# Kernel optimization log

Measured on AMD Instinct MI355X. Metric: run time of the kernel, lower is better.

Reference implementation:

```python
import jax, jax.numpy as jnp
import numpy as np

DIM = 384
NUM_HEADS = 12
HEAD_DIM = 32
MID = NUM_HEADS * HEAD_DIM
RES = (32, 32)


def _relative_position_index(res):
    Hh, Ww = res
    coords = np.stack(np.meshgrid(np.arange(Hh), np.arange(Ww), indexing='ij'))  # 2,H,W
    cf = coords.reshape(2, -1)
    rel = cf[:, :, None] - cf[:, None, :]  # 2,N,N
    rel = rel.transpose(1, 2, 0).astype(np.int64)
    rel[:, :, 0] += Hh - 1
    rel[:, :, 1] += Ww - 1
    rel[:, :, 0] *= 2 * Ww - 1
    return rel.sum(-1)  # N,N


def setup_inputs() -> dict:
    key = jax.random.key(0)
    ks = jax.random.split(key, 8)
    B = 8
    Hh, Ww = RES
    table_size = (2 * Hh - 1) * (2 * Ww - 1)
    x = jax.random.normal(ks[0], (B, DIM, Hh, Ww), dtype=jnp.float32)
    wq = jax.random.normal(ks[1], (MID, DIM), dtype=jnp.float32) * 0.02
    bq = jnp.zeros((MID,), dtype=jnp.float32)
    wkv = jax.random.normal(ks[2], (2 * MID, DIM), dtype=jnp.float32) * 0.02
    bkv = jnp.zeros((2 * MID,), dtype=jnp.float32)
    wproj = jax.random.normal(ks[3], (DIM, MID), dtype=jnp.float32) * 0.02
    bproj = jnp.zeros((DIM,), dtype=jnp.float32)
    bias_table = jax.random.normal(ks[4], (table_size, NUM_HEADS), dtype=jnp.float32) * 0.02
    rel_index = jnp.asarray(_relative_position_index(RES), dtype=jnp.int32)  # N,N
    return {"x": x, "wq": wq, "bq": bq, "wkv": wkv, "bkv": bkv,
            "wproj": wproj, "bproj": bproj, "bias_table": bias_table,
            "rel_index": rel_index}


def reference(x, wq, bq, wkv, bkv, wproj, bproj, bias_table, rel_index):
    B, C, Hh, Ww = x.shape
    N = Hh * Ww
    scale = HEAD_DIM ** -0.5
    xf = x.reshape(B, C, N)  # B,C,N
    # 1x1 convs == channelwise linear
    q = jnp.einsum('oc,bcn->bon', wq, xf) + bq[None, :, None]          # B,MID,N
    kv = jnp.einsum('oc,bcn->bon', wkv, xf) + bkv[None, :, None]       # B,2*MID,N
    q = q.reshape(B, NUM_HEADS, HEAD_DIM, N).transpose(0, 1, 3, 2)     # B,h,N,d
    kv = kv.reshape(B, 2, NUM_HEADS, HEAD_DIM, N)
    k = kv[:, 0].transpose(0, 1, 3, 2)                                  # B,h,N,d
    v = kv[:, 1].transpose(0, 1, 3, 2)                                  # B,h,N,d
    attn = jnp.einsum('bhnd,bhmd->bhnm', q, k) * scale                  # B,h,N,N
    rel_bias = bias_table[rel_index.reshape(-1)].reshape(N, N, NUM_HEADS)
    attn = attn + rel_bias.transpose(2, 0, 1)[None]                     # + h,N,N bias
    attn = jax.nn.softmax(attn, axis=-1)
    out = jnp.einsum('bhnm,bhmd->bhnd', attn, v)                        # B,h,N,d
    out = out.transpose(0, 1, 3, 2).reshape(B, MID, N)                  # B,MID,N
    out = jnp.einsum('om,bmn->bon', wproj, out) + bproj[None, :, None]  # B,DIM,N
    return out.reshape(B, C, Hh, Ww)
```

## Files before the change

kernel.cpp:

```cpp
#include <hip/hip_runtime.h>

typedef __bf16 bf16;
typedef __bf16 bf16x8 __attribute__((ext_vector_type(8)));
typedef __bf16 bf16x4 __attribute__((ext_vector_type(4)));
typedef float  f32x4  __attribute__((ext_vector_type(4)));

static constexpr int NB = 8;
static constexpr int NH = 12;
static constexpr int HD = 32;
static constexpr int NN = 1024;
static constexpr int NC = 384;

static constexpr float LOG2E = 1.4426950408889634f;
static constexpr float QSC   = (float)(0.17677669529663687 * 1.4426950408889634);

static constexpr size_t XT_N   = (size_t)NB*NN*NC;
static constexpr size_t WQKV_N = (size_t)3*NC*NC;
static constexpr size_t WP_N   = (size_t)NC*NC;
static constexpr size_t QKV_N  = (size_t)NB*NH*NN*HD;
static constexpr size_t AO_N   = (size_t)NB*NN*NC;

static constexpr size_t XT_OFF   = 0;
static constexpr size_t WQKV_OFF = XT_OFF + XT_N;
static constexpr size_t WP_OFF   = WQKV_OFF + WQKV_N;
static constexpr size_t Q_OFF    = WP_OFF + WP_N;
static constexpr size_t K_OFF    = Q_OFF + QKV_N;
static constexpr size_t V_OFF    = K_OFF + QKV_N;
static constexpr size_t AO_OFF   = V_OFF + QKV_N;
static constexpr size_t PT_OFF   = AO_OFF + AO_N;

static constexpr int PT_PER_H = 63 * 62;
static constexpr int PT_TOTAL = NH * PT_PER_H;

#define MFMA16(a,b,c) __builtin_amdgcn_mfma_f32_16x16x32_bf16(a,b,c,0,0,0)

static __device__ inline float fast_exp2(float x) {
#if __has_builtin(__builtin_amdgcn_exp2f)
    return __builtin_amdgcn_exp2f(x);
#else
    return exp2f(x);
#endif
}

__global__ __launch_bounds__(256) void cast_all_kernel(const float* __restrict__ x,
                                                       const float* __restrict__ wq,
                                                       const float* __restrict__ wkv,
                                                       const float* __restrict__ wproj,
                                                       const float* __restrict__ bias_table,
                                                       bf16* __restrict__ xt,
                                                       bf16* __restrict__ wqkv,
                                                       bf16* __restrict__ wp,
                                                       unsigned* __restrict__ PT)
{
    __shared__ bf16 T[64][68];
    const int t = threadIdx.x;
    if (blockIdx.x >= 1344) {
        const int e = (blockIdx.x - 1344) * 256 + t;
        if (e >= PT_TOTAL) return;
        const int h = e / PT_PER_H, rem = e - h * PT_PER_H;
        const int dj = rem / 62, dip = rem - dj * 62;
        bf16 lo = (bf16)(bias_table[(size_t)((dip + 1) * 63 + dj) * NH + h] * LOG2E);
        bf16 hi = (bf16)(bias_table[(size_t)(dip * 63 + dj) * NH + h] * LOG2E);
        PT[e] = (unsigned)__builtin_bit_cast(unsigned short, lo)
              | ((unsigned)__builtin_bit_cast(unsigned short, hi) << 16);
        return;
    }
    if (blockIdx.x >= 768) {
        const size_t i = ((size_t)(blockIdx.x - 768) * 256 + t) * 4;
        if (i >= WQKV_N + WP_N) return;
        const float* src; bf16* dst;
        if (i < (size_t)NC*NC)      { src = wq + i;                     dst = wqkv + i; }
        else if (i < WQKV_N)        { src = wkv + (i - (size_t)NC*NC);  dst = wqkv + i; }
        else                        { src = wproj + (i - WQKV_N);       dst = wp + (i - WQKV_N); }
        float4 v = *(const float4*)src;
        bf16x4 o; o[0] = (bf16)v.x; o[1] = (bf16)v.y; o[2] = (bf16)v.z; o[3] = (bf16)v.w;
        *(bf16x4*)dst = o;
        return;
    }
    const int bid = blockIdx.x;
    const int b = bid / 96, rem = bid % 96, ct = rem >> 4, nt = rem & 15;
    const int c0 = ct * 64, n0 = nt * 64;
    const float* Xb = x + (size_t)b * NC * NN;
    const int nl = t & 63, c4 = (t >> 6) * 4;
#pragma unroll
    for (int i = 0; i < 4; ++i) {
        const int c = c4 + i * 16;
        bf16x4 v;
#pragma unroll
        for (int j = 0; j < 4; ++j)
            v[j] = (bf16)Xb[(size_t)(c0 + c + j) * NN + n0 + nl];
        *(bf16x4*)&T[nl][c] = v;
    }
    __syncthreads();
    const int n = t >> 2;
#pragma unroll
    for (int i = 0; i < 2; ++i) {
        const int cg = (t & 3) * 8 + i * 32;
        bf16x4 a = *(const bf16x4*)&T[n][cg];
        bf16x4 bv = *(const bf16x4*)&T[n][cg + 4];
        bf16x8 vv = __builtin_shufflevector(a, bv, 0, 1, 2, 3, 4, 5, 6, 7);
        *(bf16x8*)&xt[((size_t)b * NN + n0 + n) * NC + c0 + cg] = vv;
    }
}

__global__ __launch_bounds__(256) void qkv_gemm_kernel(
    const bf16* __restrict__ W, const bf16* __restrict__ Xt,
    const float* __restrict__ bq, const float* __restrict__ bkv,
    bf16* __restrict__ Qd, bf16* __restrict__ Kd, bf16* __restrict__ Vd)
{
    __shared__ bf16 As[128][72];
    __shared__ bf16 Bs[128][72];
    const int t = threadIdx.x;
    const int w = t >> 6, lane = t & 63, g = lane >> 4, l16 = lane & 15;
    const int wm = w >> 1, wn = w & 1;
    const int n0g = blockIdx.x * 128;
    const int b = n0g >> 10, n0 = n0g & 1023;
    const int o0 = blockIdx.y * 128;
    const bf16* Xb = Xt + (size_t)b * NN * NC;

    const int sr = t >> 1, sc2 = (t & 1) * 32;

    f32x4 acc[4][4] = {};

    bf16x8 aw[4], bw[4];
#pragma unroll
    for (int i = 0; i < 4; ++i) {
        aw[i] = *(const bf16x8*)&W [(size_t)(o0 + sr) * NC + sc2 + 8*i];
        bw[i] = *(const bf16x8*)&Xb[(size_t)(n0 + sr) * NC + sc2 + 8*i];
    }

    for (int k0 = 0; k0 < NC; k0 += 64) {
        __syncthreads();
#pragma unroll
        for (int i = 0; i < 4; ++i) {
            *(bf16x8*)&As[sr][sc2 + 8*i] = aw[i];
            *(bf16x8*)&Bs[sr][sc2 + 8*i] = bw[i];
        }
        __syncthreads();
        if (k0 + 64 < NC) {
#pragma unroll
            for (int i = 0; i < 4; ++i) {
                aw[i] = *(const bf16x8*)&W [(size_t)(o0 + sr) * NC + k0 + 64 + sc2 + 8*i];
                bw[i] = *(const bf16x8*)&Xb[(size_t)(n0 + sr) * NC + k0 + 64 + sc2 + 8*i];
            }
        }
#pragma unroll
        for (int ks = 0; ks < 2; ++ks) {
            bf16x8 a[4], bb[4];
#pragma unroll
            for (int s = 0; s < 4; ++s) {
                a[s]  = *(const bf16x8*)&As[wm*64 + s*16 + l16][ks*32 + g*8];
                bb[s] = *(const bf16x8*)&Bs[wn*64 + s*16 + l16][ks*32 + g*8];
            }
#pragma unroll
            for (int sm = 0; sm < 4; ++sm)
#pragma unroll
                for (int sn = 0; sn < 4; ++sn)
                    acc[sm][sn] = MFMA16(a[sm], bb[sn], acc[sm][sn]);
        }
    }

#pragma unroll
    for (int sm = 0; sm < 4; ++sm)
#pragma unroll
    for (int sn = 0; sn < 4; ++sn) {
        const int col   = n0 + wn*64 + sn*16 + l16;
        const int obase = o0 + wm*64 + sm*16 + g*4;
        f32x4 v = acc[sm][sn];
        if (obase < 384) {
            const int hh = obase >> 5, d = obase & 31;
            bf16x4 o4;
#pragma unroll
            for (int r = 0; r < 4; ++r) o4[r] = (bf16)((v[r] + bq[obase + r]) * QSC);
            *(bf16x4*)&Qd[(((size_t)b*NH + hh)*NN + col)*HD + d] = o4;
        } else if (obase < 768) {
            const int oo = obase - 384; const int hh = oo >> 5, d = oo & 31;
            bf16x4 o4;
#pragma unroll
            for (int r = 0; r < 4; ++r) o4[r] = (bf16)(v[r] + bkv[oo + r]);
            *(bf16x4*)&Kd[(((size_t)b*NH + hh)*NN + col)*HD + d] = o4;
        } else {
            const int oo = obase - 768; const int hh = oo >> 5, d = oo & 31;
#pragma unroll
            for (int r = 0; r < 4; ++r)
                Vd[(((size_t)b*NH + hh)*HD + d + r)*NN + col] = (bf16)(v[r] + bkv[obase - 384 + r]);
        }
    }
}

__global__ __launch_bounds__(256, 4) void attn_kernel(
    const bf16* __restrict__ Qg, const bf16* __restrict__ Kg, const bf16* __restrict__ Vg,
    const unsigned* __restrict__ PT, bf16* __restrict__ AOt)
{
    __shared__ unsigned int pairTw[63][34];
    __shared__ bf16 Ks[128][40];
    __shared__ bf16 Vs[2][32][72];

    const int t = threadIdx.x;
    const int w = t >> 6, lane = t & 63, g = lane >> 4, l16 = lane & 15;

    const int bid = blockIdx.x;
    const int nid = (bid & 7) * 96 + (bid >> 3);
    const int qt = nid & 7;
    const int hb = nid >> 3;
    const int h = hb % 12, b = hb / 12;

    const bf16* Qb = Qg + ((size_t)(b*NH + h)) * NN * HD;
    const bf16* Kb = Kg + ((size_t)(b*NH + h)) * NN * HD;
    const bf16* Vb = Vg + ((size_t)(b*NH + h)) * HD * NN;

    const int kr = t >> 1, kc2 = (t & 1) * 16;
    const int vd = t >> 3, vmb = (t & 7) * 16;
    int vsub[2], vqa[2];
#pragma unroll
    for (int i = 0; i < 2; ++i) {
        const int vm = vmb + 8*i, vmm = vm & 63;
        vsub[i] = vm >> 6;
        vqa[i]  = ((vmm >> 5) & 1) * 32 + ((vmm >> 2) & 3) * 8 + ((vmm >> 4) & 1) * 4;
    }

    bf16x8 sregK[2], sregV[2];
#pragma unroll
    for (int i = 0; i < 2; ++i) {
        sregK[i] = *(const bf16x8*)&Kb[(size_t)kr * HD + kc2 + 8*i];
        sregV[i] = *(const bf16x8*)&Vb[(size_t)vd * NN + vmb + 8*i];
    }

    const int q0 = qt * 128;
    const bf16x8 qfrag0 = *(const bf16x8*)&Qb[(size_t)(q0 + w*32      + l16) * HD + g*8];
    const bf16x8 qfrag1 = *(const bf16x8*)&Qb[(size_t)(q0 + w*32 + 16 + l16) * HD + g*8];

    const unsigned* PTh = PT + (size_t)h * PT_PER_H + 4 * qt;
    for (int idx = t; idx < 63 * 34; idx += 256) {
        const int dj = idx / 34, dipl = idx - dj * 34;
        pairTw[dj][dipl] = PTh[dj * 62 + dipl];
    }

    const unsigned* twp = &pairTw[0][0];
    const int rowD1 = (l16 + 31 - 4*g) * 34;

    bf16x8 vones;
#pragma unroll
    for (int e = 0; e < 8; ++e) vones[e] = (bf16)1.0f;

    f32x4 oacc0[2] = {}, oacc1[2] = {};
    f32x4 oacc_l0 = {}, oacc_l1 = {};

    for (int ph = 0; ph < 8; ++ph) {
        __syncthreads();
#pragma unroll
        for (int i = 0; i < 2; ++i) {
            *(bf16x8*)&Ks[kr][kc2 + 8*i] = sregK[i];
            bf16x4 vlo = __builtin_shufflevector(sregV[i], sregV[i], 0, 1, 2, 3);
            bf16x4 vhi = __builtin_shufflevector(sregV[i], sregV[i], 4, 5, 6, 7);
            *(bf16x4*)&Vs[vsub[i]][vd][vqa[i]]     = vlo;
            *(bf16x4*)&Vs[vsub[i]][vd][vqa[i] + 8] = vhi;
        }
        __syncthreads();
        if (ph < 7) {
            const int m1 = (ph + 1) * 128;
#pragma unroll
            for (int i = 0; i < 2; ++i) {
                sregK[i] = *(const bf16x8*)&Kb[(size_t)(m1 + kr) * HD + kc2 + 8*i];
                sregV[i] = *(const bf16x8*)&Vb[(size_t)vd * NN + m1 + vmb + 8*i];
            }
        }

#pragma unroll
        for (int sub = 0; sub < 2; ++sub) {
            const int it = 2 * ph + sub;
            const bf16 (*Vsp)[72] = Vs[sub];
            const int dipl = w + 30 - 2*it;
            const unsigned* pD1 = twp + rowD1 + dipl;

            f32x4 b00, b01, b02, b03, b10, b12;
#pragma unroll
            for (int r = 0; r < 4; ++r) {
                const unsigned d1w = pD1[-34 * r];
                const unsigned d0w = pD1[-34 * r - 544];
                const unsigned d2w = pD1[-34 * r + 544];
                b00[r] = __uint_as_float(d1w << 16);
                b02[r] = __uint_as_float(d1w & 0xFFFF0000u);
                b01[r] = __uint_as_float(d0w << 16);
                b03[r] = __uint_as_float(d0w & 0xFFFF0000u);
                b10[r] = __uint_as_float(d2w << 16);
                b12[r] = __uint_as_float(d2w & 0xFFFF0000u);
            }
            f32x4 bacc0[4] = {b00, b01, b02, b03};
            f32x4 bacc1[4] = {b10, b00, b12, b02};

            bf16x8 pa0[2], pa1[2];
#pragma unroll
            for (int sc = 0; sc < 4; ++sc) {
                bf16x8 kf = *(const bf16x8*)&Ks[sub*64 + sc*16 + l16][g*8];
                f32x4 z0 = MFMA16(kf, qfrag0, bacc0[sc]);
                f32x4 z1 = MFMA16(kf, qfrag1, bacc1[sc]);
                const int kc = sc >> 1, hl = (sc & 1) * 4;
#pragma unroll
                for (int r = 0; r < 4; ++r) {
                    pa0[kc][hl + r] = (bf16)fast_exp2(z0[r]);
                    pa1[kc][hl + r] = (bf16)fast_exp2(z1[r]);
                }
            }

#pragma unroll
            for (int kc = 0; kc < 2; ++kc) {
#pragma unroll
                for (int ds = 0; ds < 2; ++ds) {
                    bf16x8 vf = *(const bf16x8*)&Vsp[ds*16 + l16][kc*32 + 8*g];
                    oacc0[ds] = MFMA16(pa0[kc], vf, oacc0[ds]);
                    oacc1[ds] = MFMA16(pa1[kc], vf, oacc1[ds]);
                }
                oacc_l0 = MFMA16(pa0[kc], vones, oacc_l0);
                oacc_l1 = MFMA16(pa1[kc], vones, oacc_l1);
            }
        }
    }

    float rin0[4], rin1[4];
#pragma unroll
    for (int r = 0; r < 4; ++r) {
        rin0[r] = 1.0f / oacc_l0[r];
        rin1[r] = 1.0f / oacc_l1[r];
    }

    const int nrow0 = q0 + w*32 + g*4;
#pragma unroll
    for (int ds = 0; ds < 2; ++ds) {
        const int c = h*HD + ds*16 + l16;
#pragma unroll
        for (int r = 0; r < 4; ++r) {
            AOt[((size_t)b*NN + nrow0 + r)      * NC + c] = (bf16)(oacc0[ds][r] * rin0[r]);
            AOt[((size_t)b*NN + nrow0 + 16 + r) * NC + c] = (bf16)(oacc1[ds][r] * rin1[r]);
        }
    }
}

__global__ __launch_bounds__(256) void proj_gemm_kernel(
    const bf16* __restrict__ W, const bf16* __restrict__ AOt,
    const float* __restrict__ bproj, float* __restrict__ out)
{
    __shared__ bf16 As[64][40];
    __shared__ bf16 Bs[128][40];
    const int t = threadIdx.x;
    const int w = t >> 6, lane = t & 63, g = lane >> 4, l16 = lane & 15;
    const int wm = w >> 1, wn = w & 1;
    const int n0g = blockIdx.x * 128;
    const int b = n0g >> 10, n0 = n0g & 1023;
    const int o0 = blockIdx.y * 64;
    const bf16* Ab = AOt + (size_t)b * NN * NC;

    const int ar = t >> 2, ac = (t & 3) * 8;

    f32x4 acc[2][4] = {};

    bf16x8 aw = *(const bf16x8*)&W[(size_t)(o0 + ar) * NC + ac];
    bf16x8 bw[2];
#pragma unroll
    for (int i = 0; i < 2; ++i) {
        const int s = t + i * 256, r = s >> 2, cc = (s & 3) * 8;
        bw[i] = *(const bf16x8*)&Ab[(size_t)(n0 + r) * NC + cc];
    }

    for (int k0 = 0; k0 < NC; k0 += 32) {
        __syncthreads();
        *(bf16x8*)&As[ar][ac] = aw;
#pragma unroll
        for (int i = 0; i < 2; ++i) {
            const int s = t + i * 256, r = s >> 2, cc = (s & 3) * 8;
            *(bf16x8*)&Bs[r][cc] = bw[i];
        }
        __syncthreads();
        if (k0 + 32 < NC) {
            aw = *(const bf16x8*)&W[(size_t)(o0 + ar) * NC + k0 + 32 + ac];
#pragma unroll
            for (int i = 0; i < 2; ++i) {
                const int s = t + i * 256, r = s >> 2, cc = (s & 3) * 8;
                bw[i] = *(const bf16x8*)&Ab[(size_t)(n0 + r) * NC + k0 + 32 + cc];
            }
        }
        bf16x8 a0 = *(const bf16x8*)&As[wm*32      + l16][g*8];
        bf16x8 a1 = *(const bf16x8*)&As[wm*32 + 16 + l16][g*8];
#pragma unroll
        for (int sn = 0; sn < 4; ++sn) {
            bf16x8 bf = *(const bf16x8*)&Bs[wn*64 + sn*16 + l16][g*8];
            acc[0][sn] = MFMA16(a0, bf, acc[0][sn]);
            acc[1][sn] = MFMA16(a1, bf, acc[1][sn]);
        }
    }

#pragma unroll
    for (int sm = 0; sm < 2; ++sm)
#pragma unroll
    for (int sn = 0; sn < 4; ++sn) {
        const int col   = n0 + wn*64 + sn*16 + l16;
        const int obase = o0 + wm*32 + sm*16 + g*4;
        f32x4 v = acc[sm][sn];
#pragma unroll
        for (int r = 0; r < 4; ++r)
            out[((size_t)b*NC + obase + r)*NN + col] = v[r] + bproj[obase + r];
    }
}

extern "C" void kernel_launch(void* const* d_in, const int* in_sizes, int n_in,
                              void* d_out, int out_size, void* d_ws, size_t ws_size,
                              hipStream_t stream)
{
    const float* x          = (const float*)d_in[0];
    const float* wq         = (const float*)d_in[1];
    const float* bq         = (const float*)d_in[2];
    const float* wkv        = (const float*)d_in[3];
    const float* bkv        = (const float*)d_in[4];
    const float* wproj      = (const float*)d_in[5];
    const float* bproj      = (const float*)d_in[6];
    const float* bias_table = (const float*)d_in[7];
    float* out = (float*)d_out;

    bf16* wsb  = (bf16*)d_ws;
    bf16* Xt   = wsb + XT_OFF;
    bf16* Wqkv = wsb + WQKV_OFF;
    bf16* Wp   = wsb + WP_OFF;
    bf16* Qd   = wsb + Q_OFF;
    bf16* Kd   = wsb + K_OFF;
    bf16* Vd   = wsb + V_OFF;
    bf16* AOt  = wsb + AO_OFF;
    unsigned* PT = (unsigned*)(wsb + PT_OFF);

    const int ptBlocks = (PT_TOTAL + 255) / 256;
    cast_all_kernel<<<dim3(768 + 576 + ptBlocks), 256, 0, stream>>>(
        x, wq, wkv, wproj, bias_table, Xt, Wqkv, Wp, PT);
    qkv_gemm_kernel<<<dim3(64, 9), 256, 0, stream>>>(Wqkv, Xt, bq, bkv, Qd, Kd, Vd);
    attn_kernel<<<dim3(768), 256, 0, stream>>>(Qd, Kd, Vd, PT, AOt);
    proj_gemm_kernel<<<dim3(64, 6), 256, 0, stream>>>(Wp, AOt, bproj, out);
}
```

Baseline: 64.66 us.

## Split attention key range across two warp groups with LDS reduction

Measured after the change: 131.8 us. +103.8%, slower.

```diff
diff --git a/kernel.cpp b/kernel.cpp
--- a/kernel.cpp
+++ b/kernel.cpp
@@ -188,16 +188,18 @@
     }
 }
 
-__global__ __launch_bounds__(256, 4) void attn_kernel(
+__global__ __launch_bounds__(512, 6) void attn_kernel(
     const bf16* __restrict__ Qg, const bf16* __restrict__ Kg, const bf16* __restrict__ Vg,
     const unsigned* __restrict__ PT, bf16* __restrict__ AOt)
 {
-    __shared__ unsigned int pairTw[63][34];
-    __shared__ bf16 Ks[128][40];
-    __shared__ bf16 Vs[2][32][72];
+    __shared__ __align__(16) char arena[47488];
+    bf16 (*KsH)[128][40]   = (bf16 (*)[128][40])arena;
+    bf16 (*VsH)[2][32][72] = (bf16 (*)[2][32][72])(arena + 20480);
+    unsigned (*pairTw)[34] = (unsigned (*)[34])(arena + 38912);
 
     const int t = threadIdx.x;
     const int w = t >> 6, lane = t & 63, g = lane >> 4, l16 = lane & 15;
+    const int wl = w & 3, hf = w >> 2;
 
     const int bid = blockIdx.x;
     const int nid = (bid & 7) * 96 + (bid >> 3);
@@ -209,8 +211,9 @@
     const bf16* Kb = Kg + ((size_t)(b*NH + h)) * NN * HD;
     const bf16* Vb = Vg + ((size_t)(b*NH + h)) * HD * NN;
 
-    const int kr = t >> 1, kc2 = (t & 1) * 16;
-    const int vd = t >> 3, vmb = (t & 7) * 16;
+    const int tl = t & 255, g2 = t >> 8;
+    const int kr = tl >> 1, kc2 = (tl & 1) * 16;
+    const int vd = tl >> 3, vmb = (tl & 7) * 16;
     int vsub[2], vqa[2];
 #pragma unroll
     for (int i = 0; i < 2; ++i) {
@@ -218,20 +221,21 @@
         vsub[i] = vm >> 6;
         vqa[i]  = ((vmm >> 5) & 1) * 32 + ((vmm >> 2) & 3) * 8 + ((vmm >> 4) & 1) * 4;
     }
+    const int mbase = g2 * 512;
 
     bf16x8 sregK[2], sregV[2];
 #pragma unroll
     for (int i = 0; i < 2; ++i) {
-        sregK[i] = *(const bf16x8*)&Kb[(size_t)kr * HD + kc2 + 8*i];
-        sregV[i] = *(const bf16x8*)&Vb[(size_t)vd * NN + vmb + 8*i];
+        sregK[i] = *(const bf16x8*)&Kb[(size_t)(mbase + kr) * HD + kc2 + 8*i];
+        sregV[i] = *(const bf16x8*)&Vb[(size_t)vd * NN + mbase + vmb + 8*i];
     }
 
     const int q0 = qt * 128;
-    const bf16x8 qfrag0 = *(const bf16x8*)&Qb[(size_t)(q0 + w*32      + l16) * HD + g*8];
-    const bf16x8 qfrag1 = *(const bf16x8*)&Qb[(size_t)(q0 + w*32 + 16 + l16) * HD + g*8];
+    const bf16x8 qfrag0 = *(const bf16x8*)&Qb[(size_t)(q0 + wl*32      + l16) * HD + g*8];
+    const bf16x8 qfrag1 = *(const bf16x8*)&Qb[(size_t)(q0 + wl*32 + 16 + l16) * HD + g*8];
 
     const unsigned* PTh = PT + (size_t)h * PT_PER_H + 4 * qt;
-    for (int idx = t; idx < 63 * 34; idx += 256) {
+    for (int idx = t; idx < 63 * 34; idx += 512) {
         const int dj = idx / 34, dipl = idx - dj * 34;
         pairTw[dj][dipl] = PTh[dj * 62 + dipl];
     }
@@ -246,19 +250,19 @@
     f32x4 oacc0[2] = {}, oacc1[2] = {};
     f32x4 oacc_l0 = {}, oacc_l1 = {};
 
-    for (int ph = 0; ph < 8; ++ph) {
+    for (int ph = 0; ph < 4; ++ph) {
         __syncthreads();
 #pragma unroll
         for (int i = 0; i < 2; ++i) {
-            *(bf16x8*)&Ks[kr][kc2 + 8*i] = sregK[i];
+            *(bf16x8*)&KsH[g2][kr][kc2 + 8*i] = sregK[i];
             bf16x4 vlo = __builtin_shufflevector(sregV[i], sregV[i], 0, 1, 2, 3);
             bf16x4 vhi = __builtin_shufflevector(sregV[i], sregV[i], 4, 5, 6, 7);
-            *(bf16x4*)&Vs[vsub[i]][vd][vqa[i]]     = vlo;
-            *(bf16x4*)&Vs[vsub[i]][vd][vqa[i] + 8] = vhi;
-        }
-        __syncthreads();
-        if (ph < 7) {
-            const int m1 = (ph + 1) * 128;
+            *(bf16x4*)&VsH[g2][vsub[i]][vd][vqa[i]]     = vlo;
+            *(bf16x4*)&VsH[g2][vsub[i]][vd][vqa[i] + 8] = vhi;
+        }
+        __syncthreads();
+        if (ph < 3) {
+            const int m1 = mbase + (ph + 1) * 128;
 #pragma unroll
             for (int i = 0; i < 2; ++i) {
                 sregK[i] = *(const bf16x8*)&Kb[(size_t)(m1 + kr) * HD + kc2 + 8*i];
@@ -268,9 +272,9 @@
 
 #pragma unroll
         for (int sub = 0; sub < 2; ++sub) {
-            const int it = 2 * ph + sub;
-            const bf16 (*Vsp)[72] = Vs[sub];
-            const int dipl = w + 30 - 2*it;
+            const int it = hf * 8 + 2 * ph + sub;
+            const bf16 (*Vsp)[72] = VsH[hf][sub];
+            const int dipl = wl + 30 - 2*it;
             const unsigned* pD1 = twp + rowD1 + dipl;
 
             f32x4 b00, b01, b02, b03, b10, b12;
@@ -292,7 +296,7 @@
             bf16x8 pa0[2], pa1[2];
 #pragma unroll
             for (int sc = 0; sc < 4; ++sc) {
-                bf16x8 kf = *(const bf16x8*)&Ks[sub*64 + sc*16 + l16][g*8];
+                bf16x8 kf = *(const bf16x8*)&KsH[hf][sub*64 + sc*16 + l16][g*8];
                 f32x4 z0 = MFMA16(kf, qfrag0, bacc0[sc]);
                 f32x4 z1 = MFMA16(kf, qfrag1, bacc1[sc]);
                 const int kc = sc >> 1, hl = (sc & 1) * 4;
@@ -317,21 +321,35 @@
         }
     }
 
-    float rin0[4], rin1[4];
-#pragma unroll
-    for (int r = 0; r < 4; ++r) {
-        rin0[r] = 1.0f / oacc_l0[r];
-        rin1[r] = 1.0f / oacc_l1[r];
-    }
-
-    const int nrow0 = q0 + w*32 + g*4;
-#pragma unroll
-    for (int ds = 0; ds < 2; ++ds) {
-        const int c = h*HD + ds*16 + l16;
+    __syncthreads();
+    f32x4* mbuf = (f32x4*)arena;
+    const int sb = wl * 64 + lane;
+    if (hf == 1) {
+        mbuf[0*256 + sb] = oacc0[0]; mbuf[1*256 + sb] = oacc0[1];
+        mbuf[2*256 + sb] = oacc1[0]; mbuf[3*256 + sb] = oacc1[1];
+        mbuf[4*256 + sb] = oacc_l0;  mbuf[5*256 + sb] = oacc_l1;
+    }
+    __syncthreads();
+    if (hf == 0) {
+        oacc0[0] += mbuf[0*256 + sb]; oacc0[1] += mbuf[1*256 + sb];
+        oacc1[0] += mbuf[2*256 + sb]; oacc1[1] += mbuf[3*256 + sb];
+        oacc_l0  += mbuf[4*256 + sb]; oacc_l1  += mbuf[5*256 + sb];
+
+        float rin0[4], rin1[4];
 #pragma unroll
         for (int r = 0; r < 4; ++r) {
-            AOt[((size_t)b*NN + nrow0 + r)      * NC + c] = (bf16)(oacc0[ds][r] * rin0[r]);
-            AOt[((size_t)b*NN + nrow0 + 16 + r) * NC + c] = (bf16)(oacc1[ds][r] * rin1[r]);
+            rin0[r] = 1.0f / oacc_l0[r];
+            rin1[r] = 1.0f / oacc_l1[r];
+        }
+        const int nrow0 = q0 + wl*32 + g*4;
+#pragma unroll
+        for (int ds = 0; ds < 2; ++ds) {
+            const int c = h*HD + ds*16 + l16;
+#pragma unroll
+            for (int r = 0; r < 4; ++r) {
+                AOt[((size_t)b*NN + nrow0 + r)      * NC + c] = (bf16)(oacc0[ds][r] * rin0[r]);
+                AOt[((size_t)b*NN + nrow0 + 16 + r) * NC + c] = (bf16)(oacc1[ds][r] * rin1[r]);
+            }
         }
     }
 }
@@ -430,6 +448,6 @@
     cast_all_kernel<<<dim3(768 + 576 + ptBlocks), 256, 0, stream>>>(
         x, wq, wkv, wproj, bias_table, Xt, Wqkv, Wp, PT);
     qkv_gemm_kernel<<<dim3(64, 9), 256, 0, stream>>>(Wqkv, Xt, bq, bkv, Qd, Kd, Vd);
-    attn_kernel<<<dim3(768), 256, 0, stream>>>(Qd, Kd, Vd, PT, AOt);
+    attn_kernel<<<dim3(768), 512, 0, stream>>>(Qd, Kd, Vd, PT, AOt);
     proj_gemm_kernel<<<dim3(64, 6), 256, 0, stream>>>(Wp, AOt, bproj, out);
 }
```

## Drop LDS K/V staging in attention; read pre-permuted V directly from global

Applied to the files above, without the earlier changes.

Result: slower. 106.5 us (+64.7%).

```diff
diff --git a/kernel.cpp b/kernel.cpp
--- a/kernel.cpp
+++ b/kernel.cpp
@@ -181,9 +181,10 @@
             *(bf16x4*)&Kd[(((size_t)b*NH + hh)*NN + col)*HD + d] = o4;
         } else {
             const int oo = obase - 768; const int hh = oo >> 5, d = oo & 31;
+            const int pcol = (col & ~0x1C) | (((col >> 2) & 3) << 3) | (((col >> 4) & 1) << 2);
 #pragma unroll
             for (int r = 0; r < 4; ++r)
-                Vd[(((size_t)b*NH + hh)*HD + d + r)*NN + col] = (bf16)(v[r] + bkv[obase - 384 + r]);
+                Vd[(((size_t)b*NH + hh)*HD + d + r)*NN + pcol] = (bf16)(v[r] + bkv[obase - 384 + r]);
         }
     }
 }
@@ -192,147 +193,112 @@
     const bf16* __restrict__ Qg, const bf16* __restrict__ Kg, const bf16* __restrict__ Vg,
     const unsigned* __restrict__ PT, bf16* __restrict__ AOt)
 {
-    __shared__ unsigned int pairTw[63][34];
-    __shared__ bf16 Ks[128][40];
-    __shared__ bf16 Vs[2][32][72];
+    __shared__ unsigned pairTw[63][32];
 
     const int t = threadIdx.x;
     const int w = t >> 6, lane = t & 63, g = lane >> 4, l16 = lane & 15;
 
     const int bid = blockIdx.x;
-    const int nid = (bid & 7) * 96 + (bid >> 3);
-    const int qt = nid & 7;
-    const int hb = nid >> 3;
+    const int nid = (bid & 7) * 192 + (bid >> 3);
+    const int qt = nid & 15;
+    const int hb = nid >> 4;
     const int h = hb % 12, b = hb / 12;
 
     const bf16* Qb = Qg + ((size_t)(b*NH + h)) * NN * HD;
     const bf16* Kb = Kg + ((size_t)(b*NH + h)) * NN * HD;
     const bf16* Vb = Vg + ((size_t)(b*NH + h)) * HD * NN;
 
-    const int kr = t >> 1, kc2 = (t & 1) * 16;
-    const int vd = t >> 3, vmb = (t & 7) * 16;
-    int vsub[2], vqa[2];
-#pragma unroll
-    for (int i = 0; i < 2; ++i) {
-        const int vm = vmb + 8*i, vmm = vm & 63;
-        vsub[i] = vm >> 6;
-        vqa[i]  = ((vmm >> 5) & 1) * 32 + ((vmm >> 2) & 3) * 8 + ((vmm >> 4) & 1) * 4;
-    }
-
-    bf16x8 sregK[2], sregV[2];
-#pragma unroll
-    for (int i = 0; i < 2; ++i) {
-        sregK[i] = *(const bf16x8*)&Kb[(size_t)kr * HD + kc2 + 8*i];
-        sregV[i] = *(const bf16x8*)&Vb[(size_t)vd * NN + vmb + 8*i];
-    }
-
-    const int q0 = qt * 128;
-    const bf16x8 qfrag0 = *(const bf16x8*)&Qb[(size_t)(q0 + w*32      + l16) * HD + g*8];
-    const bf16x8 qfrag1 = *(const bf16x8*)&Qb[(size_t)(q0 + w*32 + 16 + l16) * HD + g*8];
-
-    const unsigned* PTh = PT + (size_t)h * PT_PER_H + 4 * qt;
-    for (int idx = t; idx < 63 * 34; idx += 256) {
-        const int dj = idx / 34, dipl = idx - dj * 34;
+    const int q0 = qt * 64;
+    const int n_s = q0 + w*16 + l16;
+    const bf16x8 qfrag = *(const bf16x8*)&Qb[(size_t)n_s * HD + g*8];
+
+    bf16x8 kf[2][4];
+#pragma unroll
+    for (int sc = 0; sc < 4; ++sc)
+        kf[0][sc] = *(const bf16x8*)&Kb[(size_t)(sc*16 + l16) * HD + g*8];
+
+    const unsigned* PTh = PT + (size_t)h * PT_PER_H + 2 * qt;
+    for (int idx = t; idx < 63 * 32; idx += 256) {
+        const int dj = idx >> 5, dipl = idx & 31;
         pairTw[dj][dipl] = PTh[dj * 62 + dipl];
     }
+    __syncthreads();
 
     const unsigned* twp = &pairTw[0][0];
-    const int rowD1 = (l16 + 31 - 4*g) * 34;
+    const int rowD1 = ((((w & 1) << 4) | l16) + 31 - 4*g) * 32;
 
     bf16x8 vones;
 #pragma unroll
     for (int e = 0; e < 8; ++e) vones[e] = (bf16)1.0f;
 
-    f32x4 oacc0[2] = {}, oacc1[2] = {};
-    f32x4 oacc_l0 = {}, oacc_l1 = {};
-
-    for (int ph = 0; ph < 8; ++ph) {
-        __syncthreads();
-#pragma unroll
-        for (int i = 0; i < 2; ++i) {
-            *(bf16x8*)&Ks[kr][kc2 + 8*i] = sregK[i];
-            bf16x4 vlo = __builtin_shufflevector(sregV[i], sregV[i], 0, 1, 2, 3);
-            bf16x4 vhi = __builtin_shufflevector(sregV[i], sregV[i], 4, 5, 6, 7);
-            *(bf16x4*)&Vs[vsub[i]][vd][vqa[i]]     = vlo;
-            *(bf16x4*)&Vs[vsub[i]][vd][vqa[i] + 8] = vhi;
-        }
-        __syncthreads();
-        if (ph < 7) {
-            const int m1 = (ph + 1) * 128;
-#pragma unroll
-            for (int i = 0; i < 2; ++i) {
-                sregK[i] = *(const bf16x8*)&Kb[(size_t)(m1 + kr) * HD + kc2 + 8*i];
-                sregV[i] = *(const bf16x8*)&Vb[(size_t)vd * NN + m1 + vmb + 8*i];
-            }
-        }
-
-#pragma unroll
-        for (int sub = 0; sub < 2; ++sub) {
-            const int it = 2 * ph + sub;
-            const bf16 (*Vsp)[72] = Vs[sub];
-            const int dipl = w + 30 - 2*it;
-            const unsigned* pD1 = twp + rowD1 + dipl;
-
-            f32x4 b00, b01, b02, b03, b10, b12;
-#pragma unroll
-            for (int r = 0; r < 4; ++r) {
-                const unsigned d1w = pD1[-34 * r];
-                const unsigned d0w = pD1[-34 * r - 544];
-                const unsigned d2w = pD1[-34 * r + 544];
-                b00[r] = __uint_as_float(d1w << 16);
-                b02[r] = __uint_as_float(d1w & 0xFFFF0000u);
-                b01[r] = __uint_as_float(d0w << 16);
-                b03[r] = __uint_as_float(d0w & 0xFFFF0000u);
-                b10[r] = __uint_as_float(d2w << 16);
-                b12[r] = __uint_as_float(d2w & 0xFFFF0000u);
-            }
-            f32x4 bacc0[4] = {b00, b01, b02, b03};
-            f32x4 bacc1[4] = {b10, b00, b12, b02};
-
-            bf16x8 pa0[2], pa1[2];
-#pragma unroll
-            for (int sc = 0; sc < 4; ++sc) {
-                bf16x8 kf = *(const bf16x8*)&Ks[sub*64 + sc*16 + l16][g*8];
-                f32x4 z0 = MFMA16(kf, qfrag0, bacc0[sc]);
-                f32x4 z1 = MFMA16(kf, qfrag1, bacc1[sc]);
-                const int kc = sc >> 1, hl = (sc & 1) * 4;
-#pragma unroll
-                for (int r = 0; r < 4; ++r) {
-                    pa0[kc][hl + r] = (bf16)fast_exp2(z0[r]);
-                    pa1[kc][hl + r] = (bf16)fast_exp2(z1[r]);
-                }
-            }
-
-#pragma unroll
-            for (int kc = 0; kc < 2; ++kc) {
-#pragma unroll
-                for (int ds = 0; ds < 2; ++ds) {
-                    bf16x8 vf = *(const bf16x8*)&Vsp[ds*16 + l16][kc*32 + 8*g];
-                    oacc0[ds] = MFMA16(pa0[kc], vf, oacc0[ds]);
-                    oacc1[ds] = MFMA16(pa1[kc], vf, oacc1[ds]);
-                }
-                oacc_l0 = MFMA16(pa0[kc], vones, oacc_l0);
-                oacc_l1 = MFMA16(pa1[kc], vones, oacc_l1);
-            }
-        }
-    }
-
-    float rin0[4], rin1[4];
-#pragma unroll
-    for (int r = 0; r < 4; ++r) {
-        rin0[r] = 1.0f / oacc_l0[r];
-        rin1[r] = 1.0f / oacc_l1[r];
-    }
-
-    const int nrow0 = q0 + w*32 + g*4;
+    f32x4 oacc[2] = {};
+    f32x4 oacc_l = {};
+
+#pragma unroll
+    for (int it = 0; it < 16; ++it) {
+        const int cur = it & 1, nxt = cur ^ 1;
+        const int m0 = it * 64;
+
+        bf16x8 vf[4];
+#pragma unroll
+        for (int kc = 0; kc < 2; ++kc)
+#pragma unroll
+            for (int ds = 0; ds < 2; ++ds)
+                vf[kc*2 + ds] = *(const bf16x8*)&Vb[(size_t)(ds*16 + l16) * NN + m0 + kc*32 + 8*g];
+        if (it < 15) {
+            const int m1 = m0 + 64;
+#pragma unroll
+            for (int sc = 0; sc < 4; ++sc)
+                kf[nxt][sc] = *(const bf16x8*)&Kb[(size_t)(m1 + sc*16 + l16) * HD + g*8];
+            __builtin_amdgcn_sched_group_barrier(0x20, 8, 0);
+        } else {
+            __builtin_amdgcn_sched_group_barrier(0x20, 4, 0);
+        }
+
+        const int dipl = (w >> 1) + 30 - 2*it;
+        const unsigned* pD1 = twp + rowD1 + dipl;
+
+        f32x4 bacc[4];
+#pragma unroll
+        for (int r = 0; r < 4; ++r) {
+            const unsigned prA = pD1[-32 * r];
+            const unsigned prB = pD1[-32 * r - 512];
+            bacc[0][r] = __uint_as_float(prA << 16);
+            bacc[2][r] = __uint_as_float(prA & 0xFFFF0000u);
+            bacc[1][r] = __uint_as_float(prB << 16);
+            bacc[3][r] = __uint_as_float(prB & 0xFFFF0000u);
+        }
+
+        bf16x8 pa[2];
+#pragma unroll
+        for (int sc = 0; sc < 4; ++sc) {
+            f32x4 z = MFMA16(kf[cur][sc], qfrag, bacc[sc]);
+            const int kc = sc >> 1, hl = (sc & 1) * 4;
+#pragma unroll
+            for (int r = 0; r < 4; ++r)
+                pa[kc][hl + r] = (bf16)fast_exp2(z[r]);
+        }
+
+#pragma unroll
+        for (int kc = 0; kc < 2; ++kc) {
+#pragma unroll
+            for (int ds = 0; ds < 2; ++ds)
+                oacc[ds] = MFMA16(pa[kc], vf[kc*2 + ds], oacc[ds]);
+            oacc_l = MFMA16(pa[kc], vones, oacc_l);
+        }
+    }
+
+    float rin[4];
+#pragma unroll
+    for (int r = 0; r < 4; ++r) rin[r] = 1.0f / oacc_l[r];
+
+    const int nrow = q0 + w*16 + g*4;
 #pragma unroll
     for (int ds = 0; ds < 2; ++ds) {
         const int c = h*HD + ds*16 + l16;
 #pragma unroll
-        for (int r = 0; r < 4; ++r) {
-            AOt[((size_t)b*NN + nrow0 + r)      * NC + c] = (bf16)(oacc0[ds][r] * rin0[r]);
-            AOt[((size_t)b*NN + nrow0 + 16 + r) * NC + c] = (bf16)(oacc1[ds][r] * rin1[r]);
-        }
+        for (int r = 0; r < 4; ++r)
+            AOt[((size_t)b*NN + nrow + r) * NC + c] = (bf16)(oacc[ds][r] * rin[r]);
     }
 }
 
@@ -430,6 +396,6 @@
     cast_all_kernel<<<dim3(768 + 576 + ptBlocks), 256, 0, stream>>>(
         x, wq, wkv, wproj, bias_table, Xt, Wqkv, Wp, PT);
     qkv_gemm_kernel<<<dim3(64, 9), 256, 0, stream>>>(Wqkv, Xt, bq, bkv, Qd, Kd, Vd);
-    attn_kernel<<<dim3(768), 256, 0, stream>>>(Qd, Kd, Vd, PT, AOt);
+    attn_kernel<<<dim3(1536), 256, 0, stream>>>(Qd, Kd, Vd, PT, AOt);
     proj_gemm_kernel<<<dim3(64, 6), 256, 0, stream>>>(Wp, AOt, bproj, out);
 }
```
